# Performance work log

Measured on AMD Instinct MI355X. Metric: run time of the kernel, lower is better.

## Reference

```python
import jax, jax.numpy as jnp
import numpy as np

N_NODES = 100_000
N_EDGES = 1_600_000
N_TRI = 1_000_000
HID = 64
NNZ0 = 2 * N_EDGES  # d0: 2 nonzeros per edge
NNZ1 = 3 * N_TRI    # d1: 3 nonzeros per 2-clique


def spmm(rows, cols, vals, x, n_out):
    """out[r] = sum_{k: rows[k]==r} vals[k] * x[cols[k]]  (sparse @ dense)."""
    return jax.ops.segment_sum(vals[:, None] * x[cols], rows, num_segments=n_out)


def setup_inputs() -> dict:
    key = jax.random.key(0)
    ks = jax.random.split(key, 12)
    q = jax.random.normal(ks[0], (N_NODES, HID), dtype=jnp.float32)
    p = jax.random.normal(ks[1], (N_EDGES, HID), dtype=jnp.float32)
    # attention weights used as divisors -> keep bounded away from 0
    A0 = jax.random.uniform(ks[2], (N_NODES,), jnp.float32, 0.5, 1.5)
    A1 = jax.random.uniform(ks[3], (N_EDGES,), jnp.float32, 0.5, 1.5)
    A2 = jax.random.uniform(ks[4], (N_TRI,), jnp.float32, 0.5, 1.5)
    alpha_raw = jnp.ones((1,), dtype=jnp.float32)
    d0_rows = jax.random.randint(ks[5], (NNZ0,), 0, N_EDGES, dtype=jnp.int32)
    d0_cols = jax.random.randint(ks[6], (NNZ0,), 0, N_NODES, dtype=jnp.int32)
    d0_vals = jax.random.normal(ks[7], (NNZ0,), dtype=jnp.float32)
    d1_rows = jax.random.randint(ks[8], (NNZ1,), 0, N_TRI, dtype=jnp.int32)
    d1_cols = jax.random.randint(ks[9], (NNZ1,), 0, N_EDGES, dtype=jnp.int32)
    d1_vals = jax.random.normal(ks[10], (NNZ1,), dtype=jnp.float32)
    return {
        "q": q, "p": p, "A0": A0, "A1": A1, "A2": A2, "alpha_raw": alpha_raw,
        "d0_rows": d0_rows, "d0_cols": d0_cols, "d0_vals": d0_vals,
        "d1_rows": d1_rows, "d1_cols": d1_cols, "d1_vals": d1_vals,
    }


def reference(q, p, A0, A1, A2, alpha_raw,
              d0_rows, d0_cols, d0_vals, d1_rows, d1_cols, d1_vals):
    n_nodes = q.shape[0]
    n_edges = p.shape[0]
    n_tri = A2.shape[0]
    alpha = jax.nn.sigmoid(alpha_raw)  # opt['alpha_multiplier']
    a0 = A0[:, None]  # [N,1]
    a1 = A1[:, None]  # [E,1]
    a2 = A2[:, None]  # [T,1]

    # bracket == 'gradient'
    # qPart = -alpha * d0^T (A1 * d0 (q / A0)) / A0
    d0ainvq = spmm(d0_rows, d0_cols, d0_vals, q / a0, n_edges)          # [E,H]
    qPart = -alpha * spmm(d0_cols, d0_rows, d0_vals, a1 * d0ainvq, n_nodes) / a0

    # pPart = -alpha * ( d1^T (A2 * d1 (p / A1)) / A1 + d0 (d0^T p / A0) )
    d1ainvp = spmm(d1_rows, d1_cols, d1_vals, p / a1, n_tri)            # [T,H]
    d1ad1Part = spmm(d1_cols, d1_rows, d1_vals, a2 * d1ainvp, n_edges) / a1
    a0invd0tp = spmm(d0_cols, d0_rows, d0_vals, p, n_nodes) / a0        # [N,H]
    d0d0aPart = spmm(d0_rows, d0_cols, d0_vals, a0invd0tp, n_edges)     # [E,H]
    pPart = -alpha * (d1ad1Part + d0d0aPart)

    return (qPart, pPart)
```

## Files before the change

kernel.cpp:

```cpp
#include <hip/hip_runtime.h>

#define HID 64

typedef unsigned short ushort_t;
typedef unsigned int uint_t;
typedef unsigned long long ull_t;
typedef float fx4 __attribute__((ext_vector_type(4)));

__device__ __forceinline__ ushort_t f2bf(float f) {
    uint_t u = __float_as_uint(f);
    u += 0x7FFFu + ((u >> 16) & 1u);
    return (ushort_t)(u >> 16);
}
__device__ __forceinline__ float bf2f(ushort_t h) {
    return __uint_as_float(((uint_t)h) << 16);
}

__device__ __forceinline__ void ntstore4(float* dst, float a, float b, float c, float d) {
    fx4 t; t[0] = a; t[1] = b; t[2] = c; t[3] = d;
    __builtin_nontemporal_store(t, (fx4*)dst);
}


__global__ __launch_bounds__(256) void count_rank2(
    const int* __restrict__ d0r, const int* __restrict__ d0c,
    const int* __restrict__ d1r, const int* __restrict__ d1c,
    int* __restrict__ rowcat,
    ushort2* __restrict__ rank0, ushort2* __restrict__ rank1,
    int off_d0r, int off_d0c, int off_d1r, int off_d1c,
    int nnz0, int nnz1)
{
    int b = blockIdx.x;
    int cb0 = (nnz0 + 255) >> 8;
    if (b < cb0) {
        int k = b * 256 + threadIdx.x;
        if (k < nnz0) {
            int A = d0r[k], B = d0c[k];
            int r0 = atomicAdd(&rowcat[off_d0r + A + 1], 1);
            int r1 = atomicAdd(&rowcat[off_d0c + B + 1], 1);
            ushort2 rk; rk.x = (unsigned short)r0; rk.y = (unsigned short)r1;
            rank0[k] = rk;
        }
    } else {
        int k = (b - cb0) * 256 + threadIdx.x;
        if (k < nnz1) {
            int A = d1r[k], B = d1c[k];
            int r0 = atomicAdd(&rowcat[off_d1r + A + 1], 1);
            int r1 = atomicAdd(&rowcat[off_d1c + B + 1], 1);
            ushort2 rk; rk.x = (unsigned short)r0; rk.y = (unsigned short)r1;
            rank1[k] = rk;
        }
    }
}

__global__ __launch_bounds__(256) void fill_conv(
    const int* __restrict__ d0r, const int* __restrict__ d0c,
    const float* __restrict__ v0, const float* __restrict__ A0d,
    const int* __restrict__ d1r, const int* __restrict__ d1c,
    const float* __restrict__ v1, const float* __restrict__ A1d,
    const int* __restrict__ S,
    const ushort2* __restrict__ rank0, const ushort2* __restrict__ rank1,
    int2* __restrict__ pcv,
    int off_d0r, int off_d0c, int off_d1r, int off_d1c,
    int nnz0, int nnz1,
    const float* __restrict__ p, ushort_t* __restrict__ ph, long long np,
    int nfill, int npair)
{
    int b = blockIdx.x;
    int fb = -1, vb = -1;
    if (b < 2 * npair) {
        if (b & 1) vb = b >> 1; else fb = b >> 1;
    } else {
        int rem = b - 2 * npair;
        if (nfill > npair) fb = npair + rem; else vb = npair + rem;
    }
    if (fb >= 0) {
        int cb0 = (nnz0 + 255) >> 8;
        if (fb < cb0) {
            int k = fb * 256 + threadIdx.x;
            if (k < nnz0) {
                int A = __builtin_nontemporal_load(d0r + k);
                int B = __builtin_nontemporal_load(d0c + k);
                float v = __builtin_nontemporal_load(v0 + k);
                ushort2 rk = rank0[k];
                int2 ea; ea.x = B; ea.y = __float_as_int(v / A0d[B]);
                pcv[S[off_d0r + A] + rk.x] = ea;
                int2 eb; eb.x = A; eb.y = __float_as_int(v);
                pcv[S[off_d0c + B] + rk.y] = eb;
            }
        } else {
            int k = (fb - cb0) * 256 + threadIdx.x;
            if (k < nnz1) {
                int A = __builtin_nontemporal_load(d1r + k);
                int B = __builtin_nontemporal_load(d1c + k);
                float v = __builtin_nontemporal_load(v1 + k);
                ushort2 rk = rank1[k];
                int2 ea; ea.x = B; ea.y = __float_as_int(v / A1d[B]);
                pcv[S[off_d1r + A] + rk.x] = ea;
                int2 eb; eb.x = A; eb.y = __float_as_int(v);
                pcv[S[off_d1c + B] + rk.y] = eb;
            }
        }
    } else {
        const fx4* p4 = (const fx4*)p;
        ushort4* h4p = (ushort4*)ph;
        long long nf4 = np >> 2;
        long long f0 = (long long)vb * 1024 + threadIdx.x;
#pragma unroll
        for (int c = 0; c < 4; ++c) {
            long long f = f0 + c * 256;
            if (f < nf4) {
                fx4 v = __builtin_nontemporal_load(p4 + f);
                ushort4 o;
                o.x = f2bf(v[0]); o.y = f2bf(v[1]); o.z = f2bf(v[2]); o.w = f2bf(v[3]);
                h4p[f] = o;
            }
        }
    }
}

#define SCAN_TPB 256
#define SCAN_IPT 32
#define SCAN_TILE (SCAN_TPB * SCAN_IPT)

__global__ __launch_bounds__(256) void scan1(int* __restrict__ data,
                                             int* __restrict__ blockSums, int n) {
    __shared__ int sdata[SCAN_TPB];
    int base = blockIdx.x * SCAN_TILE + threadIdx.x * SCAN_IPT;
    int v[SCAN_IPT];
    int s = 0;
#pragma unroll
    for (int i = 0; i < SCAN_IPT; ++i) {
        int idx = base + i;
        int x = (idx < n) ? data[idx] : 0;
        s += x;
        v[i] = s;
    }
    sdata[threadIdx.x] = s;
    __syncthreads();
    for (int off = 1; off < SCAN_TPB; off <<= 1) {
        int t = (threadIdx.x >= off) ? sdata[threadIdx.x - off] : 0;
        __syncthreads();
        sdata[threadIdx.x] += t;
        __syncthreads();
    }
    int excl = (threadIdx.x == 0) ? 0 : sdata[threadIdx.x - 1];
#pragma unroll
    for (int i = 0; i < SCAN_IPT; ++i) {
        int idx = base + i;
        if (idx < n) data[idx] = v[i] + excl;
    }
    if (threadIdx.x == SCAN_TPB - 1) blockSums[blockIdx.x] = sdata[SCAN_TPB - 1];
}

__global__ __launch_bounds__(1024) void scan2(int* __restrict__ blockSums, int nb) {
    __shared__ int sdata[1024];
    int x = (threadIdx.x < nb) ? blockSums[threadIdx.x] : 0;
    sdata[threadIdx.x] = x;
    __syncthreads();
    for (int off = 1; off < 1024; off <<= 1) {
        int t = (threadIdx.x >= off) ? sdata[threadIdx.x - off] : 0;
        __syncthreads();
        sdata[threadIdx.x] += t;
        __syncthreads();
    }
    if (threadIdx.x < nb) blockSums[threadIdx.x] = sdata[threadIdx.x];
}

__global__ __launch_bounds__(256) void scan3(int* __restrict__ data,
                                             const int* __restrict__ blockSums, int n) {
    if (blockIdx.x == 0) return;
    int add = blockSums[blockIdx.x - 1];
    int base = blockIdx.x * SCAN_TILE + threadIdx.x;
#pragma unroll
    for (int i = 0; i < SCAN_IPT; ++i) {
        int idx = base + i * SCAN_TPB;
        if (idx < n) data[idx] += add;
    }
}


template <int SRCH>
__device__ __forceinline__ float4 gather_row(const void* __restrict__ xv, int col, int h4) {
    if constexpr (SRCH) {
        ushort4 hv = *((const ushort4*)((const ushort_t*)xv + (size_t)col * HID) + h4);
        float4 r; r.x = bf2f(hv.x); r.y = bf2f(hv.y); r.z = bf2f(hv.z); r.w = bf2f(hv.w);
        return r;
    } else {
        return *((const float4*)((const float*)xv + (size_t)col * HID) + h4);
    }
}

template <int SRCH, int OUTH>
__device__ __forceinline__ void spmm4_body(
    const int* __restrict__ rps, const int2* __restrict__ pcv,
    const void* __restrict__ xv, void* __restrict__ outv,
    const float* __restrict__ rmul, const float* __restrict__ rdiv,
    const float* __restrict__ alpha_raw, int nrows, int blk)
{
    int h4 = threadIdx.x & 15;
    int sub16 = threadIdx.x >> 4;
    int rbase = (blk * 16 + sub16) * 4;
    if (rbase >= nrows) return;
    int rp[5];
#pragma unroll
    for (int i = 0; i < 5; ++i) rp[i] = rps[min(rbase + i, nrows)];
    int len[4], last[4];
#pragma unroll
    for (int r = 0; r < 4; ++r) {
        len[r] = rp[r + 1] - rp[r];
        last[r] = max(rp[r + 1] - 1, 0);
    }
    int maxlen = max(max(len[0], len[1]), max(len[2], len[3]));
    float4 acc[4];
#pragma unroll
    for (int r = 0; r < 4; ++r) acc[r] = float4{0.f, 0.f, 0.f, 0.f};

    for (int j = 0; j < maxlen; j += 2) {
        int2 e0[4], e1[4];
#pragma unroll
        for (int r = 0; r < 4; ++r) {
            e0[r] = pcv[min(rp[r] + j, last[r])];
            e1[r] = pcv[min(rp[r] + j + 1, last[r])];
        }
        float4 g0[4], g1[4];
#pragma unroll
        for (int r = 0; r < 4; ++r) g0[r] = gather_row<SRCH>(xv, e0[r].x, h4);
#pragma unroll
        for (int r = 0; r < 4; ++r) g1[r] = gather_row<SRCH>(xv, e1[r].x, h4);
#pragma unroll
        for (int r = 0; r < 4; ++r) {
            float va = (j < len[r]) ? __int_as_float(e0[r].y) : 0.f;
            float vb = (j + 1 < len[r]) ? __int_as_float(e1[r].y) : 0.f;
            acc[r].x += va * g0[r].x + vb * g1[r].x;
            acc[r].y += va * g0[r].y + vb * g1[r].y;
            acc[r].z += va * g0[r].z + vb * g1[r].z;
            acc[r].w += va * g0[r].w + vb * g1[r].w;
        }
    }

    float sgn = alpha_raw ? -(1.0f / (1.0f + expf(-alpha_raw[0]))) : 1.0f;
#pragma unroll
    for (int r = 0; r < 4; ++r) {
        int row = rbase + r;
        if (row >= nrows) break;
        float s = sgn;
        if (rmul) s *= rmul[row];
        if (rdiv) s /= rdiv[row];
        float4 a = acc[r];
        a.x *= s; a.y *= s; a.z *= s; a.w *= s;
        if constexpr (OUTH) {
            ushort4 o;
            o.x = f2bf(a.x); o.y = f2bf(a.y); o.z = f2bf(a.z); o.w = f2bf(a.w);
            *((ushort4*)((ushort_t*)outv + (size_t)row * HID) + h4) = o;
        } else {
            ntstore4((float*)((float4*)((float*)outv + (size_t)row * HID) + h4),
                     a.x, a.y, a.z, a.w);
        }
    }
}

template <int SRCH, int OUTH>
__global__ __launch_bounds__(256) void csr_spmm4(
    const int* __restrict__ rps, const int2* __restrict__ pcv,
    const void* __restrict__ xv, void* __restrict__ outv,
    const float* __restrict__ rmul, const float* __restrict__ rdiv,
    const float* __restrict__ alpha_raw, int nrows)
{
    spmm4_body<SRCH, OUTH>(rps, pcv, xv, outv, rmul, rdiv, alpha_raw, nrows, blockIdx.x);
}

__global__ __launch_bounds__(256) void csr_spmm_dual(
    const int* __restrict__ rpsT, const int* __restrict__ rpsN,
    const int2* __restrict__ pcv, const ushort_t* __restrict__ ph,
    ushort_t* __restrict__ outT, ushort_t* __restrict__ outN,
    const float* __restrict__ a2, int n_tri, int n_nodes, int triBlocks)
{
    if ((int)blockIdx.x < triBlocks)
        spmm4_body<1, 1>(rpsT, pcv, ph, outT, a2, nullptr, nullptr, n_tri, blockIdx.x);
    else
        spmm4_body<1, 1>(rpsN, pcv, ph, outN, nullptr, nullptr, nullptr, n_nodes,
                         blockIdx.x - triBlocks);
}

__global__ __launch_bounds__(256) void csr_fused_epq(
    const int* __restrict__ rpsA, const int* __restrict__ rpsB,
    const int2* __restrict__ pcv,
    const float* __restrict__ q, const ushort_t* __restrict__ tmpn,
    const ushort_t* __restrict__ tmpt,
    const float* __restrict__ a1d, const float* __restrict__ alpha_raw,
    ushort_t* __restrict__ oute1, float* __restrict__ outp, int nrows)
{
    int h4 = threadIdx.x & 15;
    int sub16 = threadIdx.x >> 4;
    int rbase = (blockIdx.x * 16 + sub16) * 4;
    if (rbase >= nrows) return;

    int rpA[5], rpB[5];
#pragma unroll
    for (int i = 0; i < 5; ++i) {
        int idx = min(rbase + i, nrows);
        rpA[i] = rpsA[idx];
        rpB[i] = rpsB[idx];
    }
    int lA[4], lastA[4], lB[4], lastB[4];
#pragma unroll
    for (int r = 0; r < 4; ++r) {
        lA[r] = rpA[r + 1] - rpA[r]; lastA[r] = max(rpA[r + 1] - 1, 0);
        lB[r] = rpB[r + 1] - rpB[r]; lastB[r] = max(rpB[r + 1] - 1, 0);
    }
    int mA = max(max(lA[0], lA[1]), max(lA[2], lA[3]));
    int mB = max(max(lB[0], lB[1]), max(lB[2], lB[3]));

    float4 accQ[4], accN[4], accT[4];
#pragma unroll
    for (int r = 0; r < 4; ++r) {
        accQ[r] = float4{0.f, 0.f, 0.f, 0.f};
        accN[r] = float4{0.f, 0.f, 0.f, 0.f};
        accT[r] = float4{0.f, 0.f, 0.f, 0.f};
    }

    for (int j = 0; j < mA; ++j) {
        int2 e[4];
#pragma unroll
        for (int r = 0; r < 4; ++r) e[r] = pcv[min(rpA[r] + j, lastA[r])];
        float4 gq[4]; ushort4 gn[4];
#pragma unroll
        for (int r = 0; r < 4; ++r)
            gq[r] = *((const float4*)(q + (size_t)e[r].x * HID) + h4);
#pragma unroll
        for (int r = 0; r < 4; ++r)
            gn[r] = *((const ushort4*)(tmpn + (size_t)e[r].x * HID) + h4);
#pragma unroll
        for (int r = 0; r < 4; ++r) {
            float v = (j < lA[r]) ? __int_as_float(e[r].y) : 0.f;
            accQ[r].x += v * gq[r].x; accQ[r].y += v * gq[r].y;
            accQ[r].z += v * gq[r].z; accQ[r].w += v * gq[r].w;
            accN[r].x += v * bf2f(gn[r].x); accN[r].y += v * bf2f(gn[r].y);
            accN[r].z += v * bf2f(gn[r].z); accN[r].w += v * bf2f(gn[r].w);
        }
    }

    for (int j = 0; j < mB; j += 2) {
        int2 e0[4], e1[4];
#pragma unroll
        for (int r = 0; r < 4; ++r) {
            e0[r] = pcv[min(rpB[r] + j, lastB[r])];
            e1[r] = pcv[min(rpB[r] + j + 1, lastB[r])];
        }
        ushort4 g0[4], g1[4];
#pragma unroll
        for (int r = 0; r < 4; ++r)
            g0[r] = *((const ushort4*)(tmpt + (size_t)e0[r].x * HID) + h4);
#pragma unroll
        for (int r = 0; r < 4; ++r)
            g1[r] = *((const ushort4*)(tmpt + (size_t)e1[r].x * HID) + h4);
#pragma unroll
        for (int r = 0; r < 4; ++r) {
            float va = (j < lB[r]) ? __int_as_float(e0[r].y) : 0.f;
            float vb = (j + 1 < lB[r]) ? __int_as_float(e1[r].y) : 0.f;
            accT[r].x += va * bf2f(g0[r].x) + vb * bf2f(g1[r].x);
            accT[r].y += va * bf2f(g0[r].y) + vb * bf2f(g1[r].y);
            accT[r].z += va * bf2f(g0[r].z) + vb * bf2f(g1[r].z);
            accT[r].w += va * bf2f(g0[r].w) + vb * bf2f(g1[r].w);
        }
    }

    float ns = -(1.0f / (1.0f + expf(-alpha_raw[0])));
#pragma unroll
    for (int r = 0; r < 4; ++r) {
        int row = rbase + r;
        if (row >= nrows) break;
        float a1v = a1d[row];
        ushort4 o;
        o.x = f2bf(accQ[r].x * a1v); o.y = f2bf(accQ[r].y * a1v);
        o.z = f2bf(accQ[r].z * a1v); o.w = f2bf(accQ[r].w * a1v);
        *((ushort4*)(oute1 + (size_t)row * HID) + h4) = o;
        float ia = 1.0f / a1v;
        ntstore4((float*)((float4*)(outp + (size_t)row * HID) + h4),
                 ns * (accN[r].x + accT[r].x * ia),
                 ns * (accN[r].y + accT[r].y * ia),
                 ns * (accN[r].z + accT[r].z * ia),
                 ns * (accN[r].w + accT[r].w * ia));
    }
}


__global__ __launch_bounds__(256) void count_rows(const int* __restrict__ ridx,
                                                  int* __restrict__ rowptr, int nnz) {
    int k = blockIdx.x * 256 + threadIdx.x;
    if (k < nnz) atomicAdd(&rowptr[ridx[k] + 1], 1);
}

__global__ __launch_bounds__(256) void copy_int(const int* __restrict__ src,
                                                int* __restrict__ dst, int n) {
    int i = blockIdx.x * 256 + threadIdx.x;
    if (i < n) dst[i] = src[i];
}

__global__ __launch_bounds__(256) void fill_csr(const int* __restrict__ ridx,
                                                const int* __restrict__ cidx,
                                                const float* __restrict__ vals,
                                                int* __restrict__ cursor,
                                                int2* __restrict__ pcv, int nnz) {
    int k = blockIdx.x * 256 + threadIdx.x;
    if (k >= nnz) return;
    int pos = atomicAdd(&cursor[ridx[k]], 1);
    int2 e;
    e.x = cidx[k];
    e.y = __float_as_int(vals[k]);
    pcv[pos] = e;
}

template <int SRCH, int OUTH>
__global__ __launch_bounds__(256) void csr_spmm_t(
    const int* __restrict__ rowptr, const int2* __restrict__ pcv,
    const void* __restrict__ xv, void* __restrict__ outv,
    const float* __restrict__ gdiag, int gdiv,
    const float* __restrict__ rmul,
    const float* __restrict__ rdiv,
    const float* __restrict__ alpha_raw,
    int nrows)
{
    int lane = threadIdx.x & 63;
    int wave = threadIdx.x >> 6;
    int sub = lane >> 4;
    int h4 = lane & 15;
    int row = blockIdx.x * 16 + wave * 4 + sub;
    if (row >= nrows) return;
    int start = rowptr[row], end = rowptr[row + 1];
    float4 acc = {0.f, 0.f, 0.f, 0.f};
    for (int j = start; j < end; ++j) {
        int2 e = pcv[j];
        int c = e.x;
        float v = __int_as_float(e.y);
        if (gdiag) { float t = gdiag[c]; v = gdiv ? v / t : v * t; }
        float4 xvv = gather_row<SRCH>(xv, c, h4);
        acc.x += v * xvv.x; acc.y += v * xvv.y; acc.z += v * xvv.z; acc.w += v * xvv.w;
    }
    float s = 1.0f;
    if (rmul) s *= rmul[row];
    if (rdiv) s /= rdiv[row];
    if (alpha_raw) s *= -(1.0f / (1.0f + expf(-alpha_raw[0])));
    acc.x *= s; acc.y *= s; acc.z *= s; acc.w *= s;
    if constexpr (OUTH) {
        ushort_t* out = (ushort_t*)outv;
        ushort4 o;
        o.x = f2bf(acc.x); o.y = f2bf(acc.y); o.z = f2bf(acc.z); o.w = f2bf(acc.w);
        *((ushort4*)(out + (size_t)row * HID) + h4) = o;
    } else {
        float* out = (float*)outv;
        *((float4*)(out + (size_t)row * HID) + h4) = acc;
    }
}

template <int BH>
__global__ __launch_bounds__(256) void csr_spmm_fused_t(
    const int* __restrict__ rowptrA, const int2* __restrict__ pcvA, const float* __restrict__ xA,
    const int* __restrict__ rowptrB, const int2* __restrict__ pcvB, const void* __restrict__ xBv,
    const float* __restrict__ a1, const float* __restrict__ alpha_raw,
    float* __restrict__ out, int nrows)
{
    int lane = threadIdx.x & 63;
    int wave = threadIdx.x >> 6;
    int sub = lane >> 4;
    int h4 = lane & 15;
    int row = blockIdx.x * 16 + wave * 4 + sub;
    if (row >= nrows) return;

    float4 accA = {0.f, 0.f, 0.f, 0.f};
    {
        int start = rowptrA[row], end = rowptrA[row + 1];
        for (int j = start; j < end; ++j) {
            int2 e = pcvA[j];
            float v = __int_as_float(e.y);
            const float4 xv = *((const float4*)(xA + (size_t)e.x * HID) + h4);
            accA.x += v * xv.x; accA.y += v * xv.y; accA.z += v * xv.z; accA.w += v * xv.w;
        }
    }
    float4 accB = {0.f, 0.f, 0.f, 0.f};
    {
        int start = rowptrB[row], end = rowptrB[row + 1];
        for (int j = start; j < end; ++j) {
            int2 e = pcvB[j];
            float v = __int_as_float(e.y);
            float4 xv = gather_row<BH>(xBv, e.x, h4);
            accB.x += v * xv.x; accB.y += v * xv.y; accB.z += v * xv.z; accB.w += v * xv.w;
        }
    }
    float inv_a1 = 1.0f / a1[row];
    float ns = -(1.0f / (1.0f + expf(-alpha_raw[0])));
    float4 r;
    r.x = ns * (accA.x + accB.x * inv_a1);
    r.y = ns * (accA.y + accB.y * inv_a1);
    r.z = ns * (accA.z + accB.z * inv_a1);
    r.w = ns * (accA.w + accB.w * inv_a1);
    *((float4*)(out + (size_t)row * HID) + h4) = r;
}

__global__ __launch_bounds__(256) void spmm_scatter(
    const int* __restrict__ gidx, const int* __restrict__ sidx,
    const float* __restrict__ vals, const float* __restrict__ x,
    float* __restrict__ out,
    const float* __restrict__ gscale, int ginv,
    const float* __restrict__ sscale, int sinv,
    const float* __restrict__ alpha_raw, int nnz)
{
    int k = (blockIdx.x << 2) | (threadIdx.x >> 6);
    if (k >= nnz) return;
    int h = threadIdx.x & 63;
    int g = gidx[k];
    int s = sidx[k];
    float f = vals[k];
    if (gscale) { float t = gscale[g]; f = ginv ? (f / t) : (f * t); }
    if (sscale) { float t = sscale[s]; f = sinv ? (f / t) : (f * t); }
    if (alpha_raw) {
        float sig = 1.0f / (1.0f + expf(-alpha_raw[0]));
        f = -f * sig;
    }
    atomicAdd(out + (size_t)s * HID + h, f * x[(size_t)g * HID + h]);
}


extern "C" void kernel_launch(void* const* d_in, const int* in_sizes, int n_in,
                              void* d_out, int out_size, void* d_ws, size_t ws_size,
                              hipStream_t stream) {
    const float* q         = (const float*)d_in[0];
    const float* p         = (const float*)d_in[1];
    const float* A0        = (const float*)d_in[2];
    const float* A1        = (const float*)d_in[3];
    const float* A2        = (const float*)d_in[4];
    const float* alpha_raw = (const float*)d_in[5];
    const int*   d0_rows   = (const int*)d_in[6];
    const int*   d0_cols   = (const int*)d_in[7];
    const float* d0_vals   = (const float*)d_in[8];
    const int*   d1_rows   = (const int*)d_in[9];
    const int*   d1_cols   = (const int*)d_in[10];
    const float* d1_vals   = (const float*)d_in[11];

    const int n_nodes = in_sizes[2];
    const int n_edges = in_sizes[3];
    const int n_tri   = in_sizes[4];
    const int nnz0    = in_sizes[6];
    const int nnz1    = in_sizes[9];

    float* qPart = (float*)d_out;
    float* pPart = (float*)d_out + (size_t)n_nodes * HID;

    const size_t qPartBytes = (size_t)n_nodes * HID * sizeof(float);
    const size_t pPartBytes = (size_t)n_edges * HID * sizeof(float);

    dim3 blk(256);

    const int off_d0r = 0;
    const int off_d0c = off_d0r + n_edges;
    const int off_d1r = off_d0c + n_nodes;
    const int off_d1c = off_d1r + n_tri;
    const int NR      = off_d1c + n_edges;

    {
        char* w = (char*)d_ws;
        auto alloc = [&](size_t bytes) -> char* {
            char* ptr = w;
            w += (bytes + 255) & ~(size_t)255;
            return ptr;
        };
        ushort_t* bufA   = (ushort_t*)alloc((size_t)n_edges * HID * sizeof(ushort_t));
        ushort_t* tmp_th = (ushort_t*)alloc((size_t)n_tri * HID * sizeof(ushort_t));
        ushort_t* tmp_nh = (ushort_t*)alloc((size_t)n_nodes * HID * sizeof(ushort_t));
        int*      Z      = (int*)alloc((size_t)(NR + 2) * sizeof(int));
        int*      S      = Z + 1;
        int*      blockSums = (int*)alloc(2048 * sizeof(int));
        int2*     pcvcat = (int2*)alloc(((size_t)nnz0 * 2 + (size_t)nnz1 * 2) * sizeof(int2));
        size_t rankBytes = ((size_t)nnz0 + (size_t)nnz1) * sizeof(ushort2);
        ushort2* rank0;
        if (rankBytes <= (size_t)n_tri * HID * sizeof(ushort_t))
            rank0 = (ushort2*)tmp_th;
        else
            rank0 = (ushort2*)alloc(rankBytes);
        ushort2* rank1 = rank0 + nnz0;
        size_t needed = (size_t)(w - (char*)d_ws);

        if (needed <= ws_size) {
            hipMemsetAsync(Z, 0, (size_t)(NR + 2) * sizeof(int), stream);
            int cb0 = (nnz0 + 255) / 256;
            int cb1 = (nnz1 + 255) / 256;
            count_rank2<<<cb0 + cb1, blk, 0, stream>>>(
                d0_rows, d0_cols, d1_rows, d1_cols, S, rank0, rank1,
                off_d0r, off_d0c, off_d1r, off_d1c, nnz0, nnz1);
            {
                int n = NR + 1;
                int nb = (n + SCAN_TILE - 1) / SCAN_TILE;
                scan1<<<nb, SCAN_TPB, 0, stream>>>(S, blockSums, n);
                scan2<<<1, 1024, 0, stream>>>(blockSums, nb);
                scan3<<<nb, SCAN_TPB, 0, stream>>>(S, blockSums, n);
            }
            long long np = (long long)n_edges * HID;
            int cbc = (int)((np / 4 + 1023) / 1024);
            int nfill = cb0 + cb1;
            int npair = min(nfill, cbc);
            fill_conv<<<nfill + cbc, blk, 0, stream>>>(
                d0_rows, d0_cols, d0_vals, A0,
                d1_rows, d1_cols, d1_vals, A1,
                S, rank0, rank1, pcvcat,
                off_d0r, off_d0c, off_d1r, off_d1c, nnz0, nnz1,
                p, bufA, np, nfill, npair);

            int triB  = (n_tri + 63) / 64;
            int nodeB = (n_nodes + 63) / 64;
            int edgeB = (n_edges + 63) / 64;

            csr_spmm_dual<<<triB + nodeB, blk, 0, stream>>>(
                S + off_d1r, S + off_d0c, pcvcat, bufA, tmp_th, tmp_nh,
                A2, n_tri, n_nodes, triB);

            csr_fused_epq<<<edgeB, blk, 0, stream>>>(
                S + off_d0r, S + off_d1c, pcvcat, q, tmp_nh, tmp_th,
                A1, alpha_raw, bufA, pPart, n_edges);

            csr_spmm4<1, 0><<<nodeB, blk, 0, stream>>>(
                S + off_d0c, pcvcat, bufA, qPart, nullptr, A0, alpha_raw, n_nodes);
            return;
        }
    }

    {
        char* w = (char*)d_ws;
        auto alloc = [&](size_t bytes) -> char* {
            char* ptr = w;
            w += (bytes + 255) & ~(size_t)255;
            return ptr;
        };
        float* tmp_t = (float*)alloc((size_t)n_tri * HID * sizeof(float));
        float* tmp_n = (float*)alloc((size_t)n_nodes * HID * sizeof(float));
        size_t rpTotal = (size_t)(n_edges + 1) + (n_nodes + 1) + (n_tri + 1) + (n_edges + 1);
        int* rpBase = (int*)alloc(rpTotal * sizeof(int));
        int* rp_d0r = rpBase;
        int* rp_d0c = rp_d0r + (n_edges + 1);
        int* rp_d1r = rp_d0c + (n_nodes + 1);
        int* rp_d1c = rp_d1r + (n_tri + 1);
        int nmax = n_edges > n_tri ? n_edges : n_tri;
        if (n_nodes > nmax) nmax = n_nodes;
        int* cursor    = (int*)alloc((size_t)nmax * sizeof(int));
        int* blockSums = (int*)alloc(2048 * sizeof(int));
        int2* pcv_d0r = (int2*)alloc((size_t)nnz0 * sizeof(int2));
        int2* pcv_d0c = (int2*)alloc((size_t)nnz0 * sizeof(int2));
        int2* pcv_d1r = (int2*)alloc((size_t)nnz1 * sizeof(int2));
        int2* pcv_d1c = (int2*)alloc((size_t)nnz1 * sizeof(int2));
        size_t needed = (size_t)(w - (char*)d_ws);

        if (needed <= ws_size) {
            hipMemsetAsync(rpBase, 0, rpTotal * sizeof(int), stream);
            dim3 gk0((nnz0 + 255) / 256);
            dim3 gk1((nnz1 + 255) / 256);
            count_rows<<<gk0, blk, 0, stream>>>(d0_rows, rp_d0r, nnz0);
            count_rows<<<gk0, blk, 0, stream>>>(d0_cols, rp_d0c, nnz0);
            count_rows<<<gk1, blk, 0, stream>>>(d1_rows, rp_d1r, nnz1);
            count_rows<<<gk1, blk, 0, stream>>>(d1_cols, rp_d1c, nnz1);

            struct Build {
                int* rowptr; int nout; const int* ridx; const int* cidx; const float* vals;
                int2* pcv; int nnz;
            } builds[4] = {
                { rp_d0r, n_edges, d0_rows, d0_cols, d0_vals, pcv_d0r, nnz0 },
                { rp_d0c, n_nodes, d0_cols, d0_rows, d0_vals, pcv_d0c, nnz0 },
                { rp_d1r, n_tri,   d1_rows, d1_cols, d1_vals, pcv_d1r, nnz1 },
                { rp_d1c, n_edges, d1_cols, d1_rows, d1_vals, pcv_d1c, nnz1 },
            };
            for (int b = 0; b < 4; ++b) {
                int n = builds[b].nout + 1;
                int nb = (n + SCAN_TILE - 1) / SCAN_TILE;
                scan1<<<nb, SCAN_TPB, 0, stream>>>(builds[b].rowptr, blockSums, n);
                scan2<<<1, 1024, 0, stream>>>(blockSums, nb);
                scan3<<<nb, SCAN_TPB, 0, stream>>>(builds[b].rowptr, blockSums, n);
                copy_int<<<(builds[b].nout + 255) / 256, blk, 0, stream>>>(
                    builds[b].rowptr, cursor, builds[b].nout);
                fill_csr<<<(builds[b].nnz + 255) / 256, blk, 0, stream>>>(
                    builds[b].ridx, builds[b].cidx, builds[b].vals, cursor,
                    builds[b].pcv, builds[b].nnz);
            }

            float* tmp_e1 = pPart;
            csr_spmm_t<0, 0><<<(n_edges + 15) / 16, blk, 0, stream>>>(
                rp_d0r, pcv_d0r, q, tmp_e1, A0, 1, A1, nullptr, nullptr, n_edges);
            csr_spmm_t<0, 0><<<(n_nodes + 15) / 16, blk, 0, stream>>>(
                rp_d0c, pcv_d0c, tmp_e1, qPart, nullptr, 0, nullptr, A0, alpha_raw, n_nodes);
            csr_spmm_t<0, 0><<<(n_tri + 15) / 16, blk, 0, stream>>>(
                rp_d1r, pcv_d1r, p, tmp_t, A1, 1, A2, nullptr, nullptr, n_tri);
            csr_spmm_t<0, 0><<<(n_nodes + 15) / 16, blk, 0, stream>>>(
                rp_d0c, pcv_d0c, p, tmp_n, nullptr, 0, nullptr, A0, nullptr, n_nodes);
            csr_spmm_fused_t<0><<<(n_edges + 15) / 16, blk, 0, stream>>>(
                rp_d0r, pcv_d0r, tmp_n,
                rp_d1c, pcv_d1c, tmp_t,
                A1, alpha_raw, pPart, n_edges);
            return;
        }
    }

    {
        float* tmp = (float*)d_ws;
        const size_t triBytes  = (size_t)n_tri * HID * sizeof(float);
        const size_t nodeBytes = qPartBytes;
        dim3 g0((nnz0 + 3) / 4);
        dim3 g1((nnz1 + 3) / 4);
        hipMemsetAsync(qPart, 0, qPartBytes, stream);
        hipMemsetAsync(pPart, 0, pPartBytes, stream);
        spmm_scatter<<<g0, blk, 0, stream>>>(d0_cols, d0_rows, d0_vals, q, pPart,
                                             A0, 1, nullptr, 0, nullptr, nnz0);
        spmm_scatter<<<g0, blk, 0, stream>>>(d0_rows, d0_cols, d0_vals, pPart, qPart,
                                             A1, 0, A0, 1, alpha_raw, nnz0);
        hipMemsetAsync(pPart, 0, pPartBytes, stream);
        hipMemsetAsync(tmp, 0, triBytes, stream);
        spmm_scatter<<<g1, blk, 0, stream>>>(d1_cols, d1_rows, d1_vals, p, tmp,
                                             A1, 1, nullptr, 0, nullptr, nnz1);
        spmm_scatter<<<g1, blk, 0, stream>>>(d1_rows, d1_cols, d1_vals, tmp, pPart,
                                             A2, 0, A1, 1, alpha_raw, nnz1);
        hipMemsetAsync(tmp, 0, nodeBytes, stream);
        spmm_scatter<<<g0, blk, 0, stream>>>(d0_rows, d0_cols, d0_vals, p, tmp,
                                             nullptr, 0, A0, 1, nullptr, nnz0);
        spmm_scatter<<<g0, blk, 0, stream>>>(d0_cols, d0_rows, d0_vals, tmp, pPart,
                                             nullptr, 0, nullptr, 0, alpha_raw, nnz0);
    }
}
```

Baseline: 1.984 ms.

## Shard CSR fill scatter by destination row across XCD-mapped blocks, shrink ranks to bytes

The fill kernel now launches eight blocks per nnz chunk, one per shard (shard = blockIdx & 7), and each block writes only the entries whose destination row falls in its shard. Blocks are assigned round-robin to XCDs, so this aims to keep each XCD's scatter writes into pcv within one slice of the array, which should improve L2 locality. Per-entry ranks are stored as 8-bit bytes in four separate arrays instead of ushort2, which cuts rank traffic. The costs are that the index arrays are read eight times, and ranks are truncated to 8 bits, which gives wrong results for any row with more than 255 nonzeros.

```diff
diff --git a/kernel.cpp b/kernel.cpp
--- a/kernel.cpp
+++ b/kernel.cpp
@@ -4,6 +4,7 @@
 
 typedef unsigned short ushort_t;
 typedef unsigned int uint_t;
+typedef unsigned char uchar_t;
 typedef unsigned long long ull_t;
 typedef float fx4 __attribute__((ext_vector_type(4)));
 
@@ -21,12 +22,17 @@
     __builtin_nontemporal_store(t, (fx4*)dst);
 }
 
-
-__global__ __launch_bounds__(256) void count_rank2(
+__device__ __forceinline__ int shard_of(int row, uint_t scale) {
+    return (int)(((ull_t)(uint_t)row * scale) >> 32);
+}
+
+
+__global__ __launch_bounds__(256) void count_rank8(
     const int* __restrict__ d0r, const int* __restrict__ d0c,
     const int* __restrict__ d1r, const int* __restrict__ d1c,
     int* __restrict__ rowcat,
-    ushort2* __restrict__ rank0, ushort2* __restrict__ rank1,
+    uchar_t* __restrict__ rkA0, uchar_t* __restrict__ rkB0,
+    uchar_t* __restrict__ rkA1, uchar_t* __restrict__ rkB1,
     int off_d0r, int off_d0c, int off_d1r, int off_d1c,
     int nnz0, int nnz1)
 {
@@ -38,8 +44,8 @@
             int A = d0r[k], B = d0c[k];
             int r0 = atomicAdd(&rowcat[off_d0r + A + 1], 1);
             int r1 = atomicAdd(&rowcat[off_d0c + B + 1], 1);
-            ushort2 rk; rk.x = (unsigned short)r0; rk.y = (unsigned short)r1;
-            rank0[k] = rk;
+            rkA0[k] = (uchar_t)r0;
+            rkB0[k] = (uchar_t)r1;
         }
     } else {
         int k = (b - cb0) * 256 + threadIdx.x;
@@ -47,61 +53,75 @@
             int A = d1r[k], B = d1c[k];
             int r0 = atomicAdd(&rowcat[off_d1r + A + 1], 1);
             int r1 = atomicAdd(&rowcat[off_d1c + B + 1], 1);
-            ushort2 rk; rk.x = (unsigned short)r0; rk.y = (unsigned short)r1;
-            rank1[k] = rk;
-        }
-    }
-}
-
-__global__ __launch_bounds__(256) void fill_conv(
+            rkA1[k] = (uchar_t)r0;
+            rkB1[k] = (uchar_t)r1;
+        }
+    }
+}
+
+__global__ __launch_bounds__(256) void fill_conv8(
     const int* __restrict__ d0r, const int* __restrict__ d0c,
     const float* __restrict__ v0, const float* __restrict__ A0d,
     const int* __restrict__ d1r, const int* __restrict__ d1c,
     const float* __restrict__ v1, const float* __restrict__ A1d,
     const int* __restrict__ S,
-    const ushort2* __restrict__ rank0, const ushort2* __restrict__ rank1,
+    const uchar_t* __restrict__ rkA0, const uchar_t* __restrict__ rkB0,
+    const uchar_t* __restrict__ rkA1, const uchar_t* __restrict__ rkB1,
     int2* __restrict__ pcv,
     int off_d0r, int off_d0c, int off_d1r, int off_d1c,
-    int nnz0, int nnz1,
-    const float* __restrict__ p, ushort_t* __restrict__ ph, long long np,
-    int nfill, int npair)
+    uint_t scE, uint_t scN, uint_t scT,
+    int nnz0, int nnz1, int npair, int nchunks,
+    const float* __restrict__ p, ushort_t* __restrict__ ph, long long np)
 {
     int b = blockIdx.x;
-    int fb = -1, vb = -1;
-    if (b < 2 * npair) {
-        if (b & 1) vb = b >> 1; else fb = b >> 1;
+    int shard = b & 7;
+    int chunk = -1, vb = -1;
+    int lim = 9 * npair;
+    if (b < lim) {
+        int g = b / 9, pos = b - g * 9;
+        if (pos == 8) vb = g; else chunk = g;
     } else {
-        int rem = b - 2 * npair;
-        if (nfill > npair) fb = npair + rem; else vb = npair + rem;
-    }
-    if (fb >= 0) {
+        int rem = b - lim;
+        int fleft = (nchunks - npair) * 8;
+        if (rem < fleft) chunk = npair + (rem >> 3);
+        else vb = npair + (rem - fleft);
+    }
+    if (chunk >= 0) {
         int cb0 = (nnz0 + 255) >> 8;
-        if (fb < cb0) {
-            int k = fb * 256 + threadIdx.x;
+        if (chunk < cb0) {
+            int k = chunk * 256 + threadIdx.x;
             if (k < nnz0) {
-                int A = __builtin_nontemporal_load(d0r + k);
-                int B = __builtin_nontemporal_load(d0c + k);
-                float v = __builtin_nontemporal_load(v0 + k);
-                ushort2 rk = rank0[k];
-                int2 ea; ea.x = B; ea.y = __float_as_int(v / A0d[B]);
-                pcv[S[off_d0r + A] + rk.x] = ea;
-                int2 eb; eb.x = A; eb.y = __float_as_int(v);
-                pcv[S[off_d0c + B] + rk.y] = eb;
+                int A = d0r[k];
+                int B = d0c[k];
+                if (shard_of(A, scE) == shard) {
+                    float v = v0[k];
+                    int2 e; e.x = B; e.y = __float_as_int(v / A0d[B]);
+                    pcv[S[off_d0r + A] + rkA0[k]] = e;
+                }
+                if (shard_of(B, scN) == shard) {
+                    float v = v0[k];
+                    int2 e; e.x = A; e.y = __float_as_int(v);
+                    pcv[S[off_d0c + B] + rkB0[k]] = e;
+                }
             }
         } else {
-            int k = (fb - cb0) * 256 + threadIdx.x;
+            int k = (chunk - cb0) * 256 + threadIdx.x;
             if (k < nnz1) {
-                int A = __builtin_nontemporal_load(d1r + k);
-                int B = __builtin_nontemporal_load(d1c + k);
-                float v = __builtin_nontemporal_load(v1 + k);
-                ushort2 rk = rank1[k];
-                int2 ea; ea.x = B; ea.y = __float_as_int(v / A1d[B]);
-                pcv[S[off_d1r + A] + rk.x] = ea;
-                int2 eb; eb.x = A; eb.y = __float_as_int(v);
-                pcv[S[off_d1c + B] + rk.y] = eb;
+                int A = d1r[k];
+                int B = d1c[k];
+                if (shard_of(A, scT) == shard) {
+                    float v = v1[k];
+                    int2 e; e.x = B; e.y = __float_as_int(v / A1d[B]);
+                    pcv[S[off_d1r + A] + rkA1[k]] = e;
+                }
+                if (shard_of(B, scE) == shard) {
+                    float v = v1[k];
+                    int2 e; e.x = A; e.y = __float_as_int(v);
+                    pcv[S[off_d1c + B] + rkB1[k]] = e;
+                }
             }
         }
-    } else {
+    } else if (vb >= 0) {
         const fx4* p4 = (const fx4*)p;
         ushort4* h4p = (ushort4*)ph;
         long long nf4 = np >> 2;
@@ -572,21 +592,24 @@
         int*      S      = Z + 1;
         int*      blockSums = (int*)alloc(2048 * sizeof(int));
         int2*     pcvcat = (int2*)alloc(((size_t)nnz0 * 2 + (size_t)nnz1 * 2) * sizeof(int2));
-        size_t rankBytes = ((size_t)nnz0 + (size_t)nnz1) * sizeof(ushort2);
-        ushort2* rank0;
+        size_t rankBytes = 2 * ((size_t)nnz0 + (size_t)nnz1);
+        uchar_t* rkA0;
         if (rankBytes <= (size_t)n_tri * HID * sizeof(ushort_t))
-            rank0 = (ushort2*)tmp_th;
+            rkA0 = (uchar_t*)tmp_th;
         else
-            rank0 = (ushort2*)alloc(rankBytes);
-        ushort2* rank1 = rank0 + nnz0;
+            rkA0 = (uchar_t*)alloc(rankBytes);
+        uchar_t* rkB0 = rkA0 + nnz0;
+        uchar_t* rkA1 = rkB0 + nnz0;
+        uchar_t* rkB1 = rkA1 + nnz1;
         size_t needed = (size_t)(w - (char*)d_ws);
 
         if (needed <= ws_size) {
             hipMemsetAsync(Z, 0, (size_t)(NR + 2) * sizeof(int), stream);
             int cb0 = (nnz0 + 255) / 256;
             int cb1 = (nnz1 + 255) / 256;
-            count_rank2<<<cb0 + cb1, blk, 0, stream>>>(
-                d0_rows, d0_cols, d1_rows, d1_cols, S, rank0, rank1,
+            count_rank8<<<cb0 + cb1, blk, 0, stream>>>(
+                d0_rows, d0_cols, d1_rows, d1_cols, S,
+                rkA0, rkB0, rkA1, rkB1,
                 off_d0r, off_d0c, off_d1r, off_d1c, nnz0, nnz1);
             {
                 int n = NR + 1;
@@ -597,14 +620,20 @@
             }
             long long np = (long long)n_edges * HID;
             int cbc = (int)((np / 4 + 1023) / 1024);
-            int nfill = cb0 + cb1;
-            int npair = min(nfill, cbc);
-            fill_conv<<<nfill + cbc, blk, 0, stream>>>(
+            int nchunks = cb0 + cb1;
+            int npair = min(nchunks, cbc);
+            int grid = 9 * npair + 8 * (nchunks - npair) + (cbc - npair);
+            auto mksc = [](int n) -> uint_t {
+                return (uint_t)(((unsigned long long)8 << 32) / (unsigned)n);
+            };
+            fill_conv8<<<grid, blk, 0, stream>>>(
                 d0_rows, d0_cols, d0_vals, A0,
                 d1_rows, d1_cols, d1_vals, A1,
-                S, rank0, rank1, pcvcat,
-                off_d0r, off_d0c, off_d1r, off_d1c, nnz0, nnz1,
-                p, bufA, np, nfill, npair);
+                S, rkA0, rkB0, rkA1, rkB1, pcvcat,
+                off_d0r, off_d0c, off_d1r, off_d1c,
+                mksc(n_edges), mksc(n_nodes), mksc(n_tri),
+                nnz0, nnz1, npair, nchunks,
+                p, bufA, np);
 
             int triB  = (n_tri + 63) / 64;
             int nodeB = (n_nodes + 63) / 64;
```

Result: faster. 1.923 ms, median of 2 (-3.1%).
